# Kernel tuning notes

Measured on AMD Instinct MI355X. Metric: run time of the kernel, lower is better.

## Reference

```python
import jax, jax.numpy as jnp
import numpy as np

POOL_SIZES = [2, 4, 8]  # 2**(i+1) for num_scales=3
LN_EPS = 1e-5


def setup_inputs() -> dict:
    key = jax.random.key(0)
    ks = jax.random.split(key, 4)
    B, T, D, A, S = 32, 4096, 768, 128, 3
    x = jax.random.normal(ks[0], (B, T, D), dtype=jnp.float32)
    Wp = jax.random.normal(ks[1], (S, D, A), dtype=jnp.float32) * 0.02
    bp = jnp.zeros((S, A), dtype=jnp.float32)
    v = jax.random.normal(ks[2], (S, A), dtype=jnp.float32) * 0.02
    Wf = jax.random.normal(ks[3], (S * D, D), dtype=jnp.float32) * 0.02
    bf = jnp.zeros((D,), dtype=jnp.float32)
    gamma = jnp.ones((D,), dtype=jnp.float32)
    beta = jnp.zeros((D,), dtype=jnp.float32)
    return {"x": x, "Wp": Wp, "bp": bp, "v": v, "Wf": Wf, "bf": bf,
            "gamma": gamma, "beta": beta}


def reference(x, Wp, bp, v, Wf, bf, gamma, beta):
    B, T, D = x.shape
    feats = []
    for s, p in enumerate(POOL_SIZES):
        W = T // p  # T chosen divisible by all pool sizes -> no padding branch
        xw = x.reshape(B, W, p, D)
        e = jnp.tanh(jnp.einsum('bwpd,da->bwpa', xw, Wp[s]) + bp[s])
        scr = jnp.einsum('bwpa,a->bwp', e, v[s])
        a = jax.nn.softmax(scr, axis=-1)  # softmax over window positions
        wfeat = jnp.einsum('bwp,bwpd->bwd', a, xw)  # attention pool per window
        feats.append(wfeat.mean(axis=1))  # mean over windows -> [B, D]
    ms = jnp.concatenate(feats, axis=-1) @ Wf + bf  # [B, D]
    mu = ms.mean(axis=-1, keepdims=True)
    var = ms.var(axis=-1, keepdims=True)
    return (ms - mu) * jax.lax.rsqrt(var + LN_EPS) * gamma + beta
```

## Files before the change

### kernel.cpp

```cpp
#include <hip/hip_runtime.h>
#include <hip/hip_bf16.h>
#include <stdint.h>

#define B_  32
#define T_  4096
#define D_  768
#define A_  128
#define BT_ (B_ * T_)
#define LN_EPS 1e-5f

typedef __attribute__((ext_vector_type(8))) short  short8;
typedef __attribute__((ext_vector_type(4))) float  floatx4;

__device__ __forceinline__ uint32_t pack_bf16x2(float a, float b) {
    __hip_bfloat162 h = __float22bfloat162_rn(make_float2(a, b));
    union { __hip_bfloat162 h; uint32_t u; } cv; cv.h = h;
    return cv.u;
}

__device__ __forceinline__ uint16_t f2bf_rne(float f) {
    union { float f; uint32_t u; } cv; cv.f = f;
    uint32_t u = cv.u;
    return (uint16_t)((u + 0x7FFFu + ((u >> 16) & 1u)) >> 16);
}

__device__ __forceinline__ float fast_tanh(float x) {
    float e = __expf(2.f * x);
    return __fdividef(e - 1.f, e + 1.f);
}

__global__ __launch_bounds__(256)
void k_wp(const float* __restrict__ Wp, uint16_t* __restrict__ wpt) {
    int o = blockIdx.x * 256 + threadIdx.x;
    int s   = o / (A_ * D_);
    int rem = o - s * (A_ * D_);
    int a   = rem / D_;
    int d   = rem - a * D_;
    float f = Wp[(size_t)s * (D_ * A_) + d * A_ + a];
    wpt[o] = f2bf_rne(f);
}

__global__ __launch_bounds__(256, 2)
void k_proj_scr(const float* __restrict__ x, const uint16_t* __restrict__ wpt,
                const float* __restrict__ bp, const float* __restrict__ v,
                float* __restrict__ scr) {
    const int s    = blockIdx.x;
    const int tile = blockIdx.y;
    const int bt0  = tile * 128;
    const int tid  = threadIdx.x;
    const int lane = tid & 63;
    const int wave = tid >> 6;
    const int wrow = (wave >> 1) * 64;
    const int wcol = (wave & 1) * 64;
    const int l15  = lane & 15;
    const int quad = lane >> 4;

    __shared__ uint16_t xl[128][72];
    __shared__ float    scr_part[2][128];

    floatx4 acc[4][4];
#pragma unroll
    for (int i = 0; i < 4; ++i)
#pragma unroll
        for (int j = 0; j < 4; ++j) acc[i][j] = (floatx4){0.f, 0.f, 0.f, 0.f};

    const uint16_t* wps = wpt + (size_t)s * (A_ * D_);

    for (int k0 = 0; k0 < D_; k0 += 64) {
#pragma unroll
        for (int q = 0; q < 4; ++q) {
            int idx = tid + 256 * q;
            int row = idx >> 3;
            int c8  = (idx & 7) << 3;
            const float* gp = x + (size_t)(bt0 + row) * D_ + k0 + c8;
            float4 f0 = *(const float4*)gp;
            float4 f1 = *(const float4*)(gp + 4);
            uint4 pk;
            pk.x = pack_bf16x2(f0.x, f0.y);
            pk.y = pack_bf16x2(f0.z, f0.w);
            pk.z = pack_bf16x2(f1.x, f1.y);
            pk.w = pack_bf16x2(f1.z, f1.w);
            *(uint4*)&xl[row][c8] = pk;
        }
        __syncthreads();

        short8 bfrag[2][4];
#pragma unroll
        for (int kk = 0; kk < 2; ++kk)
#pragma unroll
            for (int j = 0; j < 4; ++j) {
                int n = wcol + j * 16 + l15;
                bfrag[kk][j] = *(const short8*)(wps + (size_t)n * D_ + k0 + kk * 32 + quad * 8);
            }

#pragma unroll
        for (int kk = 0; kk < 2; ++kk) {
            short8 afrag[4];
#pragma unroll
            for (int i = 0; i < 4; ++i)
                afrag[i] = *(const short8*)&xl[wrow + i * 16 + l15][kk * 32 + quad * 8];
#pragma unroll
            for (int i = 0; i < 4; ++i)
#pragma unroll
                for (int j = 0; j < 4; ++j)
                    acc[i][j] = __builtin_amdgcn_mfma_f32_16x16x32_bf16(
                        afrag[i], bfrag[kk][j], acc[i][j], 0, 0, 0);
        }
        __syncthreads();
    }

    float vj[4], bpj[4];
#pragma unroll
    for (int j = 0; j < 4; ++j) {
        int col = wcol + j * 16 + l15;
        vj[j]  = v[s * A_ + col];
        bpj[j] = bp[s * A_ + col];
    }
#pragma unroll
    for (int i = 0; i < 4; ++i) {
        float rs[4] = {0.f, 0.f, 0.f, 0.f};
#pragma unroll
        for (int j = 0; j < 4; ++j)
#pragma unroll
            for (int r = 0; r < 4; ++r)
                rs[r] += vj[j] * fast_tanh(acc[i][j][r] + bpj[j]);
#pragma unroll
        for (int r = 0; r < 4; ++r) {
            float t = rs[r];
            t += __shfl_xor(t, 1);
            t += __shfl_xor(t, 2);
            t += __shfl_xor(t, 4);
            t += __shfl_xor(t, 8);
            if (l15 == 0)
                scr_part[wave & 1][wrow + i * 16 + quad * 4 + r] = t;
        }
    }
    __syncthreads();
    if (tid < 128)
        scr[(size_t)s * BT_ + bt0 + tid] = scr_part[0][tid] + scr_part[1][tid];
}

template <int P>
__device__ __forceinline__ void softmax_win(float* wrow, int base) {
    float mx = -1e30f;
#pragma unroll
    for (int i = 0; i < P; ++i) mx = fmaxf(mx, wrow[base + i]);
    float e[P]; float sum = 0.f;
#pragma unroll
    for (int i = 0; i < P; ++i) { e[i] = __expf(wrow[base + i] - mx); sum += e[i]; }
    float sc = ((float)P / (float)T_) / sum;
#pragma unroll
    for (int i = 0; i < P; ++i) wrow[base + i] = e[i] * sc;
}

__global__ __launch_bounds__(256)
void k_pool(const float* __restrict__ x, const float* __restrict__ scr,
            float* __restrict__ feats) {
    const int b   = blockIdx.x;
    const int t0  = blockIdx.y * 128;
    const int tid = threadIdx.x;
    __shared__ float w[3][128];

    for (int i = tid; i < 384; i += 256) {
        int s = i >> 7, t = i & 127;
        w[s][t] = scr[(size_t)s * BT_ + b * T_ + t0 + t];
    }
    __syncthreads();

    if (tid < 64)       softmax_win<2>(&w[0][0], tid * 2);
    else if (tid < 96)  softmax_win<4>(&w[1][0], (tid - 64) * 4);
    else if (tid < 112) softmax_win<8>(&w[2][0], (tid - 96) * 8);
    __syncthreads();

    float a00=0,a01=0,a02=0, a10=0,a11=0,a12=0, a20=0,a21=0,a22=0;
    const float* xp = x + ((size_t)b * T_ + t0) * D_;
    for (int t = 0; t < 128; ++t) {
        float x0 = xp[t * D_ + tid];
        float x1 = xp[t * D_ + tid + 256];
        float x2 = xp[t * D_ + tid + 512];
        float w0 = w[0][t], w1 = w[1][t], w2 = w[2][t];
        a00 += w0 * x0; a01 += w0 * x1; a02 += w0 * x2;
        a10 += w1 * x0; a11 += w1 * x1; a12 += w1 * x2;
        a20 += w2 * x0; a21 += w2 * x1; a22 += w2 * x2;
    }
    atomicAdd(&feats[(0 * B_ + b) * D_ + tid      ], a00);
    atomicAdd(&feats[(0 * B_ + b) * D_ + tid + 256], a01);
    atomicAdd(&feats[(0 * B_ + b) * D_ + tid + 512], a02);
    atomicAdd(&feats[(1 * B_ + b) * D_ + tid      ], a10);
    atomicAdd(&feats[(1 * B_ + b) * D_ + tid + 256], a11);
    atomicAdd(&feats[(1 * B_ + b) * D_ + tid + 512], a12);
    atomicAdd(&feats[(2 * B_ + b) * D_ + tid      ], a20);
    atomicAdd(&feats[(2 * B_ + b) * D_ + tid + 256], a21);
    atomicAdd(&feats[(2 * B_ + b) * D_ + tid + 512], a22);
}

__global__ __launch_bounds__(256)
void k_ms(const float* __restrict__ feats, const float* __restrict__ Wf,
          float* __restrict__ ms) {
    const int dchunk = blockIdx.x;
    const int kchunk = blockIdx.y;
    const int k0  = kchunk * 72;
    const int tid = threadIdx.x;
    __shared__ float fl[32][72];

    for (int i = tid; i < 32 * 72; i += 256) {
        int bb = i / 72, kk = i - bb * 72;
        int k  = k0 + kk;
        int s  = k / D_;
        int d  = k - s * D_;
        fl[bb][kk] = feats[(size_t)(s * B_ + bb) * D_ + d];
    }
    __syncthreads();

    const int c     = dchunk * 128 + (tid & 127);
    const int brow0 = (tid >> 7) * 16;
    float acc[16];
#pragma unroll
    for (int r = 0; r < 16; ++r) acc[r] = 0.f;

    for (int kk = 0; kk < 72; ++kk) {
        float wv = Wf[(size_t)(k0 + kk) * D_ + c];
#pragma unroll
        for (int r = 0; r < 16; ++r) acc[r] += fl[brow0 + r][kk] * wv;
    }
#pragma unroll
    for (int r = 0; r < 16; ++r)
        atomicAdd(&ms[(size_t)(brow0 + r) * D_ + c], acc[r]);
}

__global__ __launch_bounds__(256)
void k_ln(const float* __restrict__ ms, const float* __restrict__ bf,
          const float* __restrict__ gamma, const float* __restrict__ beta,
          float* __restrict__ out) {
    const int b = blockIdx.x, tid = threadIdx.x;
    float vals[3]; float sum = 0.f, sq = 0.f;
#pragma unroll
    for (int c = 0; c < 3; ++c) {
        int d = tid + c * 256;
        float vv = ms[(size_t)b * D_ + d] + bf[d];
        vals[c] = vv; sum += vv; sq += vv * vv;
    }
#pragma unroll
    for (int m = 1; m < 64; m <<= 1) { sum += __shfl_xor(sum, m); sq += __shfl_xor(sq, m); }
    __shared__ float s1[4], s2[4];
    const int wave = tid >> 6;
    if ((tid & 63) == 0) { s1[wave] = sum; s2[wave] = sq; }
    __syncthreads();
    sum = s1[0] + s1[1] + s1[2] + s1[3];
    sq  = s2[0] + s2[1] + s2[2] + s2[3];
    float mu   = sum * (1.f / (float)D_);
    float var  = sq * (1.f / (float)D_) - mu * mu;
    float rstd = rsqrtf(var + LN_EPS);
#pragma unroll
    for (int c = 0; c < 3; ++c) {
        int d = tid + c * 256;
        out[(size_t)b * D_ + d] = (vals[c] - mu) * rstd * gamma[d] + beta[d];
    }
}

extern "C" void kernel_launch(void* const* d_in, const int* in_sizes, int n_in,
                              void* d_out, int out_size, void* d_ws, size_t ws_size,
                              hipStream_t stream) {
    const float* x     = (const float*)d_in[0];
    const float* Wp    = (const float*)d_in[1];
    const float* bp    = (const float*)d_in[2];
    const float* v     = (const float*)d_in[3];
    const float* Wf    = (const float*)d_in[4];
    const float* bfv   = (const float*)d_in[5];
    const float* gamma = (const float*)d_in[6];
    const float* beta  = (const float*)d_in[7];
    float* out = (float*)d_out;

    char* ws = (char*)d_ws;
    uint16_t* wpt   = (uint16_t*)ws;
    float*    scr   = (float*)(ws + 589824);
    float*    feats = (float*)(ws + 2162688);
    float*    ms    = (float*)(ws + 2457600);

    hipMemsetAsync(feats, 0, 294912 + 98304, stream);
    k_wp      <<<1152, 256, 0, stream>>>(Wp, wpt);
    k_proj_scr<<<dim3(3, 1024), 256, 0, stream>>>(x, wpt, bp, v, scr);
    k_pool    <<<dim3(B_, T_ / 128), 256, 0, stream>>>(x, scr, feats);
    k_ms      <<<dim3(6, 32), 256, 0, stream>>>(feats, Wf, ms);
    k_ln      <<<B_, 256, 0, stream>>>(ms, bfv, gamma, beta, out);
}
```

Baseline: 735.9 us.

## Fuse projection, scoring, softmax and pooling into one pass over x

Replaces the separate per-scale projection kernel and the pooling kernel with one kernel. It stages a 32-row tile of x as bf16 in shared memory, runs all three scale projections against it, computes the window softmax locally, and pools from the same shared tile. Before, x was read from HBM three times for scoring and once more for pooling; now it is read once, and the scr intermediate is gone. The Wp transpose is also rewritten to go through shared memory. The trade-off is that pooling now uses bf16-rounded x instead of fp32, and the B fragments are reloaded from global memory on every k-step.

```diff
diff --git a/kernel.cpp b/kernel.cpp
--- a/kernel.cpp
+++ b/kernel.cpp
@@ -24,6 +24,11 @@
     return (uint16_t)((u + 0x7FFFu + ((u >> 16) & 1u)) >> 16);
 }
 
+__device__ __forceinline__ float bf2f(uint16_t h) {
+    union { uint32_t u; float f; } cv; cv.u = ((uint32_t)h) << 16;
+    return cv.f;
+}
+
 __device__ __forceinline__ float fast_tanh(float x) {
     float e = __expf(2.f * x);
     return __fdividef(e - 1.f, e + 1.f);
@@ -31,99 +36,100 @@
 
 __global__ __launch_bounds__(256)
 void k_wp(const float* __restrict__ Wp, uint16_t* __restrict__ wpt) {
-    int o = blockIdx.x * 256 + threadIdx.x;
-    int s   = o / (A_ * D_);
-    int rem = o - s * (A_ * D_);
-    int a   = rem / D_;
-    int d   = rem - a * D_;
-    float f = Wp[(size_t)s * (D_ * A_) + d * A_ + a];
-    wpt[o] = f2bf_rne(f);
-}
-
-__global__ __launch_bounds__(256, 2)
-void k_proj_scr(const float* __restrict__ x, const uint16_t* __restrict__ wpt,
-                const float* __restrict__ bp, const float* __restrict__ v,
-                float* __restrict__ scr) {
-    const int s    = blockIdx.x;
-    const int tile = blockIdx.y;
-    const int bt0  = tile * 128;
+    const int sd = blockIdx.x;
+    const int s  = sd / 24;
+    const int d0 = (sd - s * 24) * 32;
+    const int a0 = blockIdx.y * 32;
+    const int tid = threadIdx.x;
+    const int r = tid >> 5, c = tid & 31;
+    __shared__ uint16_t tl[32][33];
+#pragma unroll
+    for (int i = 0; i < 4; ++i) {
+        int dl = r + i * 8;
+        tl[c][dl] = f2bf_rne(Wp[(size_t)s * (D_ * A_) + (d0 + dl) * A_ + a0 + c]);
+    }
+    __syncthreads();
+#pragma unroll
+    for (int i = 0; i < 4; ++i) {
+        int al = r + i * 8;
+        wpt[(size_t)s * (A_ * D_) + (a0 + al) * D_ + d0 + c] = tl[al][c];
+    }
+}
+
+__global__ __launch_bounds__(256, 3)
+void k_fused(const float* __restrict__ x, const uint16_t* __restrict__ wpt,
+             const float* __restrict__ bp, const float* __restrict__ v,
+             float* __restrict__ feats) {
+    const int bt0  = blockIdx.x * 32;
+    const int b    = bt0 >> 12;
     const int tid  = threadIdx.x;
     const int lane = tid & 63;
     const int wave = tid >> 6;
-    const int wrow = (wave >> 1) * 64;
+    const int wrow = (wave >> 1) * 16;
     const int wcol = (wave & 1) * 64;
     const int l15  = lane & 15;
     const int quad = lane >> 4;
 
-    __shared__ uint16_t xl[128][72];
-    __shared__ float    scr_part[2][128];
-
-    floatx4 acc[4][4];
-#pragma unroll
-    for (int i = 0; i < 4; ++i)
-#pragma unroll
-        for (int j = 0; j < 4; ++j) acc[i][j] = (floatx4){0.f, 0.f, 0.f, 0.f};
-
-    const uint16_t* wps = wpt + (size_t)s * (A_ * D_);
+    __shared__ uint16_t xl[32][776];
+    __shared__ float    scrp[2][3][32];
+    __shared__ float    wsm[3][32];
+
+    floatx4 acc[3][4];
+#pragma unroll
+    for (int s = 0; s < 3; ++s)
+#pragma unroll
+        for (int j = 0; j < 4; ++j) acc[s][j] = (floatx4){0.f, 0.f, 0.f, 0.f};
+
+    const int srow = tid >> 3;
+    const int sc8  = (tid & 7) << 3;
+    const float* gp0 = x + (size_t)(bt0 + srow) * D_ + sc8;
 
     for (int k0 = 0; k0 < D_; k0 += 64) {
-#pragma unroll
-        for (int q = 0; q < 4; ++q) {
-            int idx = tid + 256 * q;
-            int row = idx >> 3;
-            int c8  = (idx & 7) << 3;
-            const float* gp = x + (size_t)(bt0 + row) * D_ + k0 + c8;
-            float4 f0 = *(const float4*)gp;
-            float4 f1 = *(const float4*)(gp + 4);
-            uint4 pk;
-            pk.x = pack_bf16x2(f0.x, f0.y);
-            pk.y = pack_bf16x2(f0.z, f0.w);
-            pk.z = pack_bf16x2(f1.x, f1.y);
-            pk.w = pack_bf16x2(f1.z, f1.w);
-            *(uint4*)&xl[row][c8] = pk;
-        }
+        const float* gp = gp0 + k0;
+        float4 f0 = *(const float4*)gp;
+        float4 f1 = *(const float4*)(gp + 4);
+        uint4 pk;
+        pk.x = pack_bf16x2(f0.x, f0.y);
+        pk.y = pack_bf16x2(f0.z, f0.w);
+        pk.z = pack_bf16x2(f1.x, f1.y);
+        pk.w = pack_bf16x2(f1.z, f1.w);
+        *(uint4*)&xl[srow][k0 + sc8] = pk;
         __syncthreads();
 
-        short8 bfrag[2][4];
-#pragma unroll
-        for (int kk = 0; kk < 2; ++kk)
-#pragma unroll
-            for (int j = 0; j < 4; ++j) {
-                int n = wcol + j * 16 + l15;
-                bfrag[kk][j] = *(const short8*)(wps + (size_t)n * D_ + k0 + kk * 32 + quad * 8);
+        short8 af[2];
+        af[0] = *(const short8*)&xl[wrow + l15][k0 + quad * 8];
+        af[1] = *(const short8*)&xl[wrow + l15][k0 + 32 + quad * 8];
+
+#pragma unroll
+        for (int s = 0; s < 3; ++s) {
+            const uint16_t* wps = wpt + (size_t)s * (A_ * D_);
+#pragma unroll
+            for (int kk = 0; kk < 2; ++kk) {
+#pragma unroll
+                for (int j = 0; j < 4; ++j) {
+                    short8 bf = *(const short8*)(wps + (size_t)(wcol + j * 16 + l15) * D_
+                                                 + k0 + kk * 32 + quad * 8);
+                    acc[s][j] = __builtin_amdgcn_mfma_f32_16x16x32_bf16(af[kk], bf, acc[s][j], 0, 0, 0);
+                }
             }
-
-#pragma unroll
-        for (int kk = 0; kk < 2; ++kk) {
-            short8 afrag[4];
-#pragma unroll
-            for (int i = 0; i < 4; ++i)
-                afrag[i] = *(const short8*)&xl[wrow + i * 16 + l15][kk * 32 + quad * 8];
-#pragma unroll
-            for (int i = 0; i < 4; ++i)
-#pragma unroll
-                for (int j = 0; j < 4; ++j)
-                    acc[i][j] = __builtin_amdgcn_mfma_f32_16x16x32_bf16(
-                        afrag[i], bfrag[kk][j], acc[i][j], 0, 0, 0);
-        }
-        __syncthreads();
-    }
-
-    float vj[4], bpj[4];
-#pragma unroll
-    for (int j = 0; j < 4; ++j) {
-        int col = wcol + j * 16 + l15;
-        vj[j]  = v[s * A_ + col];
-        bpj[j] = bp[s * A_ + col];
-    }
-#pragma unroll
-    for (int i = 0; i < 4; ++i) {
+        }
+    }
+
+#pragma unroll
+    for (int s = 0; s < 3; ++s) {
+        float vj[4], bj[4];
+#pragma unroll
+        for (int j = 0; j < 4; ++j) {
+            int col = wcol + j * 16 + l15;
+            vj[j] = v[s * A_ + col];
+            bj[j] = bp[s * A_ + col];
+        }
         float rs[4] = {0.f, 0.f, 0.f, 0.f};
 #pragma unroll
         for (int j = 0; j < 4; ++j)
 #pragma unroll
             for (int r = 0; r < 4; ++r)
-                rs[r] += vj[j] * fast_tanh(acc[i][j][r] + bpj[j]);
+                rs[r] += vj[j] * fast_tanh(acc[s][j][r] + bj[j]);
 #pragma unroll
         for (int r = 0; r < 4; ++r) {
             float t = rs[r];
@@ -132,66 +138,48 @@
             t += __shfl_xor(t, 4);
             t += __shfl_xor(t, 8);
             if (l15 == 0)
-                scr_part[wave & 1][wrow + i * 16 + quad * 4 + r] = t;
-        }
-    }
-    __syncthreads();
-    if (tid < 128)
-        scr[(size_t)s * BT_ + bt0 + tid] = scr_part[0][tid] + scr_part[1][tid];
-}
-
-template <int P>
-__device__ __forceinline__ void softmax_win(float* wrow, int base) {
-    float mx = -1e30f;
-#pragma unroll
-    for (int i = 0; i < P; ++i) mx = fmaxf(mx, wrow[base + i]);
-    float e[P]; float sum = 0.f;
-#pragma unroll
-    for (int i = 0; i < P; ++i) { e[i] = __expf(wrow[base + i] - mx); sum += e[i]; }
-    float sc = ((float)P / (float)T_) / sum;
-#pragma unroll
-    for (int i = 0; i < P; ++i) wrow[base + i] = e[i] * sc;
-}
-
-__global__ __launch_bounds__(256)
-void k_pool(const float* __restrict__ x, const float* __restrict__ scr,
-            float* __restrict__ feats) {
-    const int b   = blockIdx.x;
-    const int t0  = blockIdx.y * 128;
-    const int tid = threadIdx.x;
-    __shared__ float w[3][128];
-
-    for (int i = tid; i < 384; i += 256) {
-        int s = i >> 7, t = i & 127;
-        w[s][t] = scr[(size_t)s * BT_ + b * T_ + t0 + t];
-    }
-    __syncthreads();
-
-    if (tid < 64)       softmax_win<2>(&w[0][0], tid * 2);
-    else if (tid < 96)  softmax_win<4>(&w[1][0], (tid - 64) * 4);
-    else if (tid < 112) softmax_win<8>(&w[2][0], (tid - 96) * 8);
-    __syncthreads();
-
-    float a00=0,a01=0,a02=0, a10=0,a11=0,a12=0, a20=0,a21=0,a22=0;
-    const float* xp = x + ((size_t)b * T_ + t0) * D_;
-    for (int t = 0; t < 128; ++t) {
-        float x0 = xp[t * D_ + tid];
-        float x1 = xp[t * D_ + tid + 256];
-        float x2 = xp[t * D_ + tid + 512];
-        float w0 = w[0][t], w1 = w[1][t], w2 = w[2][t];
-        a00 += w0 * x0; a01 += w0 * x1; a02 += w0 * x2;
-        a10 += w1 * x0; a11 += w1 * x1; a12 += w1 * x2;
-        a20 += w2 * x0; a21 += w2 * x1; a22 += w2 * x2;
-    }
-    atomicAdd(&feats[(0 * B_ + b) * D_ + tid      ], a00);
-    atomicAdd(&feats[(0 * B_ + b) * D_ + tid + 256], a01);
-    atomicAdd(&feats[(0 * B_ + b) * D_ + tid + 512], a02);
-    atomicAdd(&feats[(1 * B_ + b) * D_ + tid      ], a10);
-    atomicAdd(&feats[(1 * B_ + b) * D_ + tid + 256], a11);
-    atomicAdd(&feats[(1 * B_ + b) * D_ + tid + 512], a12);
-    atomicAdd(&feats[(2 * B_ + b) * D_ + tid      ], a20);
-    atomicAdd(&feats[(2 * B_ + b) * D_ + tid + 256], a21);
-    atomicAdd(&feats[(2 * B_ + b) * D_ + tid + 512], a22);
+                scrp[wave & 1][s][wrow + quad * 4 + r] = t;
+        }
+    }
+    __syncthreads();
+
+    if (tid < 28) {
+        int s, p, w0;
+        if (tid < 16)      { s = 0; p = 2; w0 = tid * 2; }
+        else if (tid < 24) { s = 1; p = 4; w0 = (tid - 16) * 4; }
+        else               { s = 2; p = 8; w0 = (tid - 24) * 8; }
+        float mx = -1e30f;
+        for (int i = 0; i < p; ++i)
+            mx = fmaxf(mx, scrp[0][s][w0 + i] + scrp[1][s][w0 + i]);
+        float e[8]; float sum = 0.f;
+        for (int i = 0; i < p; ++i) {
+            e[i] = __expf(scrp[0][s][w0 + i] + scrp[1][s][w0 + i] - mx);
+            sum += e[i];
+        }
+        float sc = ((float)p / (float)T_) / sum;
+        for (int i = 0; i < p; ++i) wsm[s][w0 + i] = e[i] * sc;
+    }
+    __syncthreads();
+
+    float pa[3][3];
+#pragma unroll
+    for (int s = 0; s < 3; ++s)
+#pragma unroll
+        for (int c = 0; c < 3; ++c) pa[s][c] = 0.f;
+    for (int t = 0; t < 32; ++t) {
+        float x0 = bf2f(xl[t][tid]);
+        float x1 = bf2f(xl[t][tid + 256]);
+        float x2 = bf2f(xl[t][tid + 512]);
+        float w0 = wsm[0][t], w1 = wsm[1][t], w2 = wsm[2][t];
+        pa[0][0] += w0 * x0; pa[0][1] += w0 * x1; pa[0][2] += w0 * x2;
+        pa[1][0] += w1 * x0; pa[1][1] += w1 * x1; pa[1][2] += w1 * x2;
+        pa[2][0] += w2 * x0; pa[2][1] += w2 * x1; pa[2][2] += w2 * x2;
+    }
+#pragma unroll
+    for (int s = 0; s < 3; ++s)
+#pragma unroll
+        for (int c = 0; c < 3; ++c)
+            atomicAdd(&feats[(size_t)(s * B_ + b) * D_ + tid + c * 256], pa[s][c]);
 }
 
 __global__ __launch_bounds__(256)
@@ -273,14 +261,12 @@
 
     char* ws = (char*)d_ws;
     uint16_t* wpt   = (uint16_t*)ws;
-    float*    scr   = (float*)(ws + 589824);
-    float*    feats = (float*)(ws + 2162688);
-    float*    ms    = (float*)(ws + 2457600);
+    float*    feats = (float*)(ws + 589824);
+    float*    ms    = (float*)(ws + 884736);
 
     hipMemsetAsync(feats, 0, 294912 + 98304, stream);
-    k_wp      <<<1152, 256, 0, stream>>>(Wp, wpt);
-    k_proj_scr<<<dim3(3, 1024), 256, 0, stream>>>(x, wpt, bp, v, scr);
-    k_pool    <<<dim3(B_, T_ / 128), 256, 0, stream>>>(x, scr, feats);
-    k_ms      <<<dim3(6, 32), 256, 0, stream>>>(feats, Wf, ms);
-    k_ln      <<<B_, 256, 0, stream>>>(ms, bfv, gamma, beta, out);
-}
+    k_wp   <<<dim3(72, 4), 256, 0, stream>>>(Wp, wpt);
+    k_fused<<<BT_ / 32, 256, 0, stream>>>(x, wpt, bp, v, feats);
+    k_ms   <<<dim3(6, 32), 256, 0, stream>>>(feats, Wf, ms);
+    k_ln   <<<B_, 256, 0, stream>>>(ms, bfv, gamma, beta, out);
+}
```

Result: slower. 1.011 ms (+37.3%).
